# Kernel tuning notes

Hardware: AMD Instinct MI355X
Metric: run time of the kernel (lower is better)

The kernel has to match this reference:

```python
import jax, jax.numpy as jnp
import numpy as np

B, N, D, H = 8, 2048, 1024, 1024

def setup_inputs() -> dict:
    key = jax.random.key(0)
    ks = jax.random.split(key, 7)
    s = 1.0 / np.sqrt(D)
    return {
        "x": jax.random.normal(ks[0], (B, N, D), dtype=jnp.float32),
        "Wq": jax.random.uniform(ks[1], (D, H), jnp.float32, -s, s),
        "bq": jax.random.uniform(ks[2], (H,), jnp.float32, -s, s),
        "Wk": jax.random.uniform(ks[3], (D, H), jnp.float32, -s, s),
        "bk": jax.random.uniform(ks[4], (H,), jnp.float32, -s, s),
        "Wv": jax.random.uniform(ks[5], (D, H), jnp.float32, -s, s),
        "bv": jax.random.uniform(ks[6], (H,), jnp.float32, -s, s),
    }

def reference(x, Wq, bq, Wk, bk, Wv, bv):
    # q, k, v: [B, N, H]
    q = jnp.einsum('bnd,dh->bnh', x, Wq) + bq
    k = jnp.einsum('bnd,dh->bnh', x, Wk) + bk
    v = jnp.einsum('bnd,dh->bnh', x, Wv) + bv
    scale = 1.0 / jnp.sqrt(jnp.asarray(q.shape[-1], q.dtype))
    score = jnp.einsum('bqh,bkh->bqk', q, k) * scale  # [B, N, N]
    causal = jnp.tril(jnp.ones((q.shape[1], q.shape[1]), dtype=bool))
    score = jnp.where(causal, score, -jnp.inf)
    attn = jax.nn.softmax(score, axis=-1)
    # dropout p=0.0 -> identity (deterministic reference)
    return jnp.einsum('bqk,bkh->bqh', attn, v)
```

## Files before the change

### kernel.cpp

```cpp
#include <hip/hip_runtime.h>
#include <hip/hip_bf16.h>
#include <stdint.h>

#define BB 8
#define NN 2048
#define DD 1024
#define HH 1024

using f32x4 = __attribute__((ext_vector_type(4))) float;
using s16x8 = __attribute__((ext_vector_type(8))) short;

__device__ __forceinline__ short f2bf(float f){
  union { float f; uint32_t u; } v; v.f = f;
  uint32_t r = (v.u + 0x7fffu + ((v.u >> 16) & 1u)) >> 16;
  return (short)r;
}
__device__ __forceinline__ float bf2f(short s){
  union { uint32_t u; float f; } v; v.u = ((uint32_t)(uint16_t)s) << 16; return v.f;
}

#define MFMA(a,b,c) __builtin_amdgcn_mfma_f32_16x16x32_bf16((a),(b),(c),0,0,0)

#define GL16(gp, lp) __builtin_amdgcn_global_load_lds( \
    (const __attribute__((address_space(1))) void*)(gp), \
    (__attribute__((address_space(3))) void*)(lp), 16, 0, 0)

__global__ __launch_bounds__(256) void k_conv_x(const float* __restrict__ x,
                                                short* __restrict__ xb){
  int gid = blockIdx.x*256 + threadIdx.x;
  const float4* xv = (const float4*)x;
  float4 a = xv[(size_t)gid*2], b2 = xv[(size_t)gid*2+1];
  s16x8 o;
  o[0]=f2bf(a.x);  o[1]=f2bf(a.y);  o[2]=f2bf(a.z);  o[3]=f2bf(a.w);
  o[4]=f2bf(b2.x); o[5]=f2bf(b2.y); o[6]=f2bf(b2.z); o[7]=f2bf(b2.w);
  *(s16x8*)(xb + (size_t)gid*8) = o;
}

__global__ __launch_bounds__(256) void k_conv_w(const float* __restrict__ Wq,
                                                const float* __restrict__ Wk,
                                                const float* __restrict__ Wv,
                                                short* __restrict__ Wt){
  __shared__ float tile[64][65];
  int bx = blockIdx.x; int mat = bx >> 8; int ti = bx & 255;
  int d0 = (ti >> 4) << 6, h0 = (ti & 15) << 6;
  const float* W = (mat==0) ? Wq : (mat==1 ? Wk : Wv);
  int t = threadIdx.x;
  for (int i=0;i<16;i++){ int e = i*256 + t; int r = e>>6, c = e&63;
    tile[r][c] = W[(size_t)(d0+r)*HH + h0 + c]; }
  __syncthreads();
  for (int i=0;i<16;i++){ int e = i*256 + t; int r = e>>6, c = e&63;
    Wt[(size_t)(mat*HH + h0 + r)*DD + d0 + c] = f2bf(tile[c][r]); }
}

__global__ __launch_bounds__(512,2) void k_gemm(const short* __restrict__ Aw,
                                                const short* __restrict__ Bw,
                                                const float* __restrict__ bq,
                                                const float* __restrict__ bk,
                                                const float* __restrict__ bv,
                                                short* __restrict__ Qw,
                                                short* __restrict__ Kw,
                                                short* __restrict__ Vt){
  __shared__ short Al[4][256*32];
  __shared__ short Bl[4][256*32];
  const int t = threadIdx.x, l = t & 63, w = t >> 6;
  const int g = l >> 4, c = l & 15;
  const int bid = blockIdx.x;
  const int bm = (bid & 7)*8 + ((bid >> 3) & 7);
  const int bn = bid >> 6;
  const int m0 = bm << 8, c0 = bn << 8;
  const int wr = w >> 2, wc = w & 3;
  f32x4 acc[8][4] = {};

  const int sr = t >> 2, sch = t & 3;
  const int u0 = sch ^ ((sr >> 1) & 3);
  const int u1 = sch ^ (((sr + 128) >> 1) & 3);
  const short* A0 = Aw + (size_t)(m0 + sr)*DD + u0*8;
  const short* A1 = Aw + (size_t)(m0 + sr + 128)*DD + u1*8;
  const short* B0 = Bw + (size_t)(c0 + sr)*DD + u0*8;
  const short* B1 = Bw + (size_t)(c0 + sr + 128)*DD + u1*8;
  const int d0b = sr*64 + sch*16, d1b = (sr+128)*64 + sch*16;
  auto stage = [&](int kt){
    int s = kt & 3, ko = kt*32;
    GL16(A0 + ko, (char*)&Al[s][0] + d0b);
    GL16(A1 + ko, (char*)&Al[s][0] + d1b);
    GL16(B0 + ko, (char*)&Bl[s][0] + d0b);
    GL16(B1 + ko, (char*)&Bl[s][0] + d1b);
  };

  int aoff[8], boff[4];
  #pragma unroll
  for (int mi=0;mi<8;mi++){
    int row = wr*128 + mi*16 + c;
    aoff[mi] = row*32 + (g ^ ((row>>1)&3))*8;
  }
  #pragma unroll
  for (int ni=0;ni<4;ni++){
    int row = wc*64 + ni*16 + c;
    boff[ni] = row*32 + (g ^ ((row>>1)&3))*8;
  }

  auto body = [&](int kt, bool dostage){
    int s = kt & 3;
    __builtin_amdgcn_sched_barrier(0);
    __builtin_amdgcn_s_barrier();
    __builtin_amdgcn_sched_barrier(0);
    s16x8 bfr[4], af[8];
    #pragma unroll
    for (int ni=0;ni<4;ni++) bfr[ni] = *(const s16x8*)&Bl[s][boff[ni]];
    #pragma unroll
    for (int mi=0;mi<8;mi++) af[mi] = *(const s16x8*)&Al[s][aoff[mi]];
    if (dostage) stage(kt+3);
    __builtin_amdgcn_s_setprio(1);
    #pragma unroll
    for (int mi=0;mi<8;mi++)
      #pragma unroll
      for (int ni=0;ni<4;ni++)
        acc[mi][ni] = MFMA(bfr[ni], af[mi], acc[mi][ni]);
    __builtin_amdgcn_s_setprio(0);
  };

  stage(0); stage(1); stage(2);
  for (int kt = 0; kt < 30; ++kt){
    asm volatile("s_waitcnt vmcnt(8)" ::: "memory");
    body(kt, kt < 29);
  }
  asm volatile("s_waitcnt vmcnt(4)" ::: "memory");
  body(30, false);
  asm volatile("s_waitcnt vmcnt(0)" ::: "memory");
  body(31, false);

  const int mat = bn >> 2;
  const float* bias = (mat==0) ? bq : (mat==1 ? bk : bv);
  if (mat < 2){
    short* Outp = (mat==0) ? Qw : Kw;
    #pragma unroll
    for (int ni=0;ni<4;ni++){
      int col0 = (bn & 3)*256 + wc*64 + ni*16 + g*4;
      float4 bv4 = *(const float4*)&bias[col0];
      #pragma unroll
      for (int mi=0;mi<8;mi++){
        int orow = m0 + wr*128 + mi*16 + c;
        short4 pk;
        pk.x = f2bf(acc[mi][ni][0] + bv4.x);
        pk.y = f2bf(acc[mi][ni][1] + bv4.y);
        pk.z = f2bf(acc[mi][ni][2] + bv4.z);
        pk.w = f2bf(acc[mi][ni][3] + bv4.w);
        *(short4*)&Outp[(size_t)orow*HH + col0] = pk;
      }
    }
  } else {
    short* S = (w < 4) ? ((short*)&Al[0][0] + w*4352)
                       : ((short*)&Bl[0][0] + (w-4)*4352);
    const int bb = m0 >> 11;
    const int nbase = m0 & 2047;
    const int hglob0 = (bn & 3)*256 + wc*64;
    #pragma unroll
    for (int rr = 0; rr < 2; ++rr){
      const int R = 2*wr + rr;
      asm volatile("" ::: "memory");
      #pragma unroll
      for (int ni=0;ni<4;ni++){
        int col0 = hglob0 + ni*16 + g*4;
        float4 bv4 = *(const float4*)&bias[col0];
        #pragma unroll
        for (int mi2=0;mi2<4;mi2++){
          short4 pk;
          pk.x = f2bf(acc[rr*4+mi2][ni][0] + bv4.x);
          pk.y = f2bf(acc[rr*4+mi2][ni][1] + bv4.y);
          pk.z = f2bf(acc[rr*4+mi2][ni][2] + bv4.z);
          pk.w = f2bf(acc[rr*4+mi2][ni][3] + bv4.w);
          *(short4*)&S[(mi2*16 + c)*68 + ni*16 + g*4] = pk;
        }
      }
      asm volatile("" ::: "memory");
      #pragma unroll
      for (int k=0;k<8;++k){
        int hr = (l>>3) + k*8;
        int ng = l & 7;
        s16x8 sv;
        #pragma unroll
        for (int e=0;e<8;e++) sv[e] = S[(ng*8+e)*68 + hr];
        *(s16x8*)&Vt[((size_t)bb*HH + hglob0 + hr)*NN + nbase + R*64 + ng*8] = sv;
      }
    }
  }
}

__global__ __launch_bounds__(512) void k_s(const short* __restrict__ Qw,
                                           const short* __restrict__ Kw,
                                           short* __restrict__ Pp){
  __shared__ short Ql[128*32];
  __shared__ short Kl[256*32];
  const int t = threadIdx.x, l = t & 63, w = t >> 6;
  const int g = l >> 4, c = l & 15;
  int p = blockIdx.x; int b = p & 7; int si = p >> 3;
  int tr = 0; while ((((tr+2)*(tr+2)) >> 2) <= si) tr++;
  int tcp = si - (((tr+1)*(tr+1)) >> 2);
  const float SC_EXP = 0.04508422002783268f;
  const int wq = w >> 2, wk = w & 3;
  f32x4 acc[4][4] = {};

  const int sr = t >> 2, sch = t & 3;
  const int su  = sch ^ ((sr >> 1) & 3);
  const int su2 = sch ^ (((sr + 128) >> 1) & 3);
  const short* Qs  = Qw + ((size_t)(b*NN + tr*128  + sr))*HH + su*8;
  const short* Ks0 = Kw + ((size_t)(b*NN + tcp*256 + sr))*HH + su*8;
  const short* Ks1 = Kw + ((size_t)(b*NN + tcp*256 + sr + 128))*HH + su2*8;

  const int rchunk = (g ^ ((c>>1)&3)) * 8;
  int qoff[4], koff[4];
  #pragma unroll
  for (int mi=0;mi<4;mi++) qoff[mi] = (wq*64 + mi*16 + c)*32 + rchunk;
  #pragma unroll
  for (int ni=0;ni<4;ni++) koff[ni] = (wk*64 + ni*16 + c)*32 + rchunk;

  for (int kt = 0; kt < 32; ++kt){
    int ko = kt*32;
    __syncthreads();
    GL16(Qs  + ko, (char*)Ql + t*16);
    GL16(Ks0 + ko, (char*)Kl + t*16);
    GL16(Ks1 + ko, (char*)Kl + 8192 + t*16);
    __syncthreads();
    s16x8 qf[4], kf[4];
    #pragma unroll
    for (int ni=0;ni<4;ni++) kf[ni] = *(const s16x8*)&Kl[koff[ni]];
    #pragma unroll
    for (int mi=0;mi<4;mi++) qf[mi] = *(const s16x8*)&Ql[qoff[mi]];
    #pragma unroll
    for (int mi=0;mi<4;mi++)
      #pragma unroll
      for (int ni=0;ni<4;ni++)
        acc[mi][ni] = MFMA(kf[ni], qf[mi], acc[mi][ni]);
  }

  short* Pt = Pp + ((size_t)(b*72 + si))*32768;
  #pragma unroll
  for (int ni=0;ni<4;ni++){
    int pc0 = wk*64 + ni*16 + g*4;
    #pragma unroll
    for (int mi=0;mi<4;mi++){
      int pr = wq*64 + mi*16 + c;
      short4 pk;
      #pragma unroll
      for (int i=0;i<4;i++){
        bool keep = (tcp*256 + pc0 + i) <= (tr*128 + pr);
        float pv = keep ? exp2f(acc[mi][ni][i]*SC_EXP) : 0.f;
        ((short*)&pk)[i] = f2bf(pv);
      }
      *(short4*)&Pt[pr*256 + pc0] = pk;
    }
  }
}

__global__ __launch_bounds__(512) void k_pv(const short* __restrict__ Pp,
                                            const short* __restrict__ Vt,
                                            float* __restrict__ out){
  __shared__ short Pl[128*32];
  __shared__ short Vl[256*32];
  const int t = threadIdx.x, l = t & 63, w = t >> 6;
  const int g = l >> 4, c = l & 15;
  int p = blockIdx.x;
  int r = p >> 8, j = p & 255;
  int tr = r ? (15 - (j >> 4)) : (j >> 4);
  int id = r ? (16 + (j & 15)) : (j & 15);
  int b = id & 7, hc = id >> 3;
  const short* Pb = Pp + ((size_t)(b*72 + (((tr+1)*(tr+1))>>2)))*32768;
  const int wq = w >> 2, wh = w & 3;
  f32x4 acc[4][4] = {};
  float ls[4] = {0.f,0.f,0.f,0.f};

  const int sr = t >> 2, sch = t & 3;
  const int su  = sch ^ ((sr >> 1) & 3);
  const int su2 = sch ^ (((sr + 128) >> 1) & 3);
  const short* Vs0 = Vt + ((size_t)(b*HH + hc*256 + sr))*NN + su*8;
  const short* Vs1 = Vt + ((size_t)(b*HH + hc*256 + sr + 128))*NN + su2*8;

  const int rchunk = (g ^ ((c>>1)&3)) * 8;
  int poff[4], voff[4];
  #pragma unroll
  for (int mi=0;mi<4;mi++) poff[mi] = (wq*64 + mi*16 + c)*32 + rchunk;
  #pragma unroll
  for (int ni=0;ni<4;ni++) voff[ni] = (wh*64 + ni*16 + c)*32 + rchunk;

  const int nst = (tr + 1) * 4;
  for (int kt = 0; kt < nst; ++kt){
    const short* Ps = Pb + (size_t)(kt>>3)*32768 + (kt&7)*32;
    __syncthreads();
    GL16(Ps + sr*256 + su*8, (char*)Pl + t*16);
    GL16(Vs0 + kt*32, (char*)Vl + t*16);
    GL16(Vs1 + kt*32, (char*)Vl + 8192 + t*16);
    __syncthreads();
    s16x8 pf[4], vf[4];
    #pragma unroll
    for (int ni=0;ni<4;ni++) vf[ni] = *(const s16x8*)&Vl[voff[ni]];
    #pragma unroll
    for (int mi=0;mi<4;mi++) pf[mi] = *(const s16x8*)&Pl[poff[mi]];
    #pragma unroll
    for (int mi=0;mi<4;mi++){
      #pragma unroll
      for (int e=0;e<8;e++) ls[mi] += bf2f(pf[mi][e]);
    }
    #pragma unroll
    for (int mi=0;mi<4;mi++)
      #pragma unroll
      for (int ni=0;ni<4;ni++)
        acc[mi][ni] = MFMA(vf[ni], pf[mi], acc[mi][ni]);
  }
  #pragma unroll
  for (int mi=0;mi<4;mi++){
    ls[mi] += __shfl_xor(ls[mi], 16);
    ls[mi] += __shfl_xor(ls[mi], 32);
  }
  #pragma unroll
  for (int mi=0;mi<4;mi++){
    float linv = 1.0f / ls[mi];
    int orow = tr*128 + wq*64 + mi*16 + c;
    #pragma unroll
    for (int ni=0;ni<4;ni++){
      int h0 = hc*256 + wh*64 + ni*16 + g*4;
      float4 o4;
      o4.x = acc[mi][ni][0]*linv; o4.y = acc[mi][ni][1]*linv;
      o4.z = acc[mi][ni][2]*linv; o4.w = acc[mi][ni][3]*linv;
      *(float4*)&out[((size_t)(b*NN + orow))*HH + h0] = o4;
    }
  }
}

extern "C" void kernel_launch(void* const* d_in, const int* in_sizes, int n_in,
                              void* d_out, int out_size, void* d_ws, size_t ws_size,
                              hipStream_t stream) {
  const float* x  = (const float*)d_in[0];
  const float* Wq = (const float*)d_in[1];
  const float* bq = (const float*)d_in[2];
  const float* Wk = (const float*)d_in[3];
  const float* bk = (const float*)d_in[4];
  const float* Wv = (const float*)d_in[5];
  const float* bv = (const float*)d_in[6];
  char* ws = (char*)d_ws;
  short* xb = (short*)(ws);
  short* Pp = (short*)(ws);
  short* Wt = (short*)(ws + 33554432u);
  short* Qw = (short*)(ws + 41943040u);
  short* Kw = (short*)(ws + 75497472u);
  short* Vt = (short*)(ws + 109051904u);

  k_conv_x<<<8192, 256, 0, stream>>>(x, xb);
  k_conv_w<<<768, 256, 0, stream>>>(Wq, Wk, Wv, Wt);
  k_gemm<<<768, 512, 0, stream>>>(xb, Wt, bq, bk, bv, Qw, Kw, Vt);
  k_s<<<576, 512, 0, stream>>>(Qw, Kw, Pp);
  k_pv<<<512, 512, 0, stream>>>(Pp, Vt, (float*)d_out);
}
```

Measured before the change: 280.5 us.

## Triple-buffer LDS tiles with async prefetch and single barrier in attention GEMMs

Converts the score and PV kernels from a load/sync/compute loop with two barriers per step into a 3-stage LDS ring buffer. Loads for step kt+2 are issued while step kt computes, with explicit vmcnt waits and one s_barrier per step. MFMA sections run at raised wave priority, and the launch bounds request two blocks per CU. This hides global-to-LDS latency, at the cost of triple the LDS footprint and hand-managed waitcnt correctness.

```diff
diff --git a/kernel.cpp b/kernel.cpp
--- a/kernel.cpp
+++ b/kernel.cpp
@@ -186,11 +186,11 @@
   }
 }
 
-__global__ __launch_bounds__(512) void k_s(const short* __restrict__ Qw,
-                                           const short* __restrict__ Kw,
-                                           short* __restrict__ Pp){
-  __shared__ short Ql[128*32];
-  __shared__ short Kl[256*32];
+__global__ __launch_bounds__(512,2) void k_s(const short* __restrict__ Qw,
+                                             const short* __restrict__ Kw,
+                                             short* __restrict__ Pp){
+  __shared__ short Ql[3][128*32];
+  __shared__ short Kl[3][256*32];
   const int t = threadIdx.x, l = t & 63, w = t >> 6;
   const int g = l >> 4, c = l & 15;
   int p = blockIdx.x; int b = p & 7; int si = p >> 3;
@@ -206,6 +206,12 @@
   const short* Qs  = Qw + ((size_t)(b*NN + tr*128  + sr))*HH + su*8;
   const short* Ks0 = Kw + ((size_t)(b*NN + tcp*256 + sr))*HH + su*8;
   const short* Ks1 = Kw + ((size_t)(b*NN + tcp*256 + sr + 128))*HH + su2*8;
+  auto stage = [&](int kt){
+    int s = kt % 3, ko = kt*32;
+    GL16(Qs  + ko, (char*)&Ql[s][0] + t*16);
+    GL16(Ks0 + ko, (char*)&Kl[s][0] + t*16);
+    GL16(Ks1 + ko, (char*)&Kl[s][0] + 8192 + t*16);
+  };
 
   const int rchunk = (g ^ ((c>>1)&3)) * 8;
   int qoff[4], koff[4];
@@ -214,24 +220,33 @@
   #pragma unroll
   for (int ni=0;ni<4;ni++) koff[ni] = (wk*64 + ni*16 + c)*32 + rchunk;
 
-  for (int kt = 0; kt < 32; ++kt){
-    int ko = kt*32;
-    __syncthreads();
-    GL16(Qs  + ko, (char*)Ql + t*16);
-    GL16(Ks0 + ko, (char*)Kl + t*16);
-    GL16(Ks1 + ko, (char*)Kl + 8192 + t*16);
-    __syncthreads();
+  auto body = [&](int kt, bool dostage){
+    int s = kt % 3;
+    __builtin_amdgcn_sched_barrier(0);
+    __builtin_amdgcn_s_barrier();
+    __builtin_amdgcn_sched_barrier(0);
     s16x8 qf[4], kf[4];
     #pragma unroll
-    for (int ni=0;ni<4;ni++) kf[ni] = *(const s16x8*)&Kl[koff[ni]];
-    #pragma unroll
-    for (int mi=0;mi<4;mi++) qf[mi] = *(const s16x8*)&Ql[qoff[mi]];
+    for (int ni=0;ni<4;ni++) kf[ni] = *(const s16x8*)&Kl[s][koff[ni]];
+    #pragma unroll
+    for (int mi=0;mi<4;mi++) qf[mi] = *(const s16x8*)&Ql[s][qoff[mi]];
+    if (dostage) stage(kt+2);
+    __builtin_amdgcn_s_setprio(1);
     #pragma unroll
     for (int mi=0;mi<4;mi++)
       #pragma unroll
       for (int ni=0;ni<4;ni++)
         acc[mi][ni] = MFMA(kf[ni], qf[mi], acc[mi][ni]);
-  }
+    __builtin_amdgcn_s_setprio(0);
+  };
+
+  stage(0); stage(1);
+  for (int kt = 0; kt < 31; ++kt){
+    asm volatile("s_waitcnt vmcnt(3)" ::: "memory");
+    body(kt, kt < 30);
+  }
+  asm volatile("s_waitcnt vmcnt(0)" ::: "memory");
+  body(31, false);
 
   short* Pt = Pp + ((size_t)(b*72 + si))*32768;
   #pragma unroll
@@ -252,11 +267,11 @@
   }
 }
 
-__global__ __launch_bounds__(512) void k_pv(const short* __restrict__ Pp,
-                                            const short* __restrict__ Vt,
-                                            float* __restrict__ out){
-  __shared__ short Pl[128*32];
-  __shared__ short Vl[256*32];
+__global__ __launch_bounds__(512,2) void k_pv(const short* __restrict__ Pp,
+                                              const short* __restrict__ Vt,
+                                              float* __restrict__ out){
+  __shared__ short Pl[3][128*32];
+  __shared__ short Vl[3][256*32];
   const int t = threadIdx.x, l = t & 63, w = t >> 6;
   const int g = l >> 4, c = l & 15;
   int p = blockIdx.x;
@@ -274,6 +289,13 @@
   const int su2 = sch ^ (((sr + 128) >> 1) & 3);
   const short* Vs0 = Vt + ((size_t)(b*HH + hc*256 + sr))*NN + su*8;
   const short* Vs1 = Vt + ((size_t)(b*HH + hc*256 + sr + 128))*NN + su2*8;
+  auto stage = [&](int kt){
+    int s = kt % 3;
+    const short* Ps = Pb + (size_t)(kt>>3)*32768 + (kt&7)*32;
+    GL16(Ps + sr*256 + su*8, (char*)&Pl[s][0] + t*16);
+    GL16(Vs0 + kt*32, (char*)&Vl[s][0] + t*16);
+    GL16(Vs1 + kt*32, (char*)&Vl[s][0] + 8192 + t*16);
+  };
 
   const int rchunk = (g ^ ((c>>1)&3)) * 8;
   int poff[4], voff[4];
@@ -282,30 +304,40 @@
   #pragma unroll
   for (int ni=0;ni<4;ni++) voff[ni] = (wh*64 + ni*16 + c)*32 + rchunk;
 
-  const int nst = (tr + 1) * 4;
-  for (int kt = 0; kt < nst; ++kt){
-    const short* Ps = Pb + (size_t)(kt>>3)*32768 + (kt&7)*32;
-    __syncthreads();
-    GL16(Ps + sr*256 + su*8, (char*)Pl + t*16);
-    GL16(Vs0 + kt*32, (char*)Vl + t*16);
-    GL16(Vs1 + kt*32, (char*)Vl + 8192 + t*16);
-    __syncthreads();
+  auto body = [&](int kt, bool dostage){
+    int s = kt % 3;
+    __builtin_amdgcn_sched_barrier(0);
+    __builtin_amdgcn_s_barrier();
+    __builtin_amdgcn_sched_barrier(0);
     s16x8 pf[4], vf[4];
     #pragma unroll
-    for (int ni=0;ni<4;ni++) vf[ni] = *(const s16x8*)&Vl[voff[ni]];
-    #pragma unroll
-    for (int mi=0;mi<4;mi++) pf[mi] = *(const s16x8*)&Pl[poff[mi]];
+    for (int ni=0;ni<4;ni++) vf[ni] = *(const s16x8*)&Vl[s][voff[ni]];
+    #pragma unroll
+    for (int mi=0;mi<4;mi++) pf[mi] = *(const s16x8*)&Pl[s][poff[mi]];
+    if (dostage) stage(kt+2);
     #pragma unroll
     for (int mi=0;mi<4;mi++){
       #pragma unroll
       for (int e=0;e<8;e++) ls[mi] += bf2f(pf[mi][e]);
     }
+    __builtin_amdgcn_s_setprio(1);
     #pragma unroll
     for (int mi=0;mi<4;mi++)
       #pragma unroll
       for (int ni=0;ni<4;ni++)
         acc[mi][ni] = MFMA(vf[ni], pf[mi], acc[mi][ni]);
-  }
+    __builtin_amdgcn_s_setprio(0);
+  };
+
+  const int nst = (tr + 1) * 4;
+  stage(0); stage(1);
+  for (int kt = 0; kt < nst - 1; ++kt){
+    asm volatile("s_waitcnt vmcnt(3)" ::: "memory");
+    body(kt, kt + 2 < nst);
+  }
+  asm volatile("s_waitcnt vmcnt(0)" ::: "memory");
+  body(nst - 1, false);
+
   #pragma unroll
   for (int mi=0;mi<4;mi++){
     ls[mi] += __shfl_xor(ls[mi], 16);
```

Measured after the change: 252.8 us. 1.11x faster.
